# Performance work log

Measured on AMD Instinct MI355X. Metric: run time of the kernel, lower is better.

Reference implementation:

```python
import jax, jax.numpy as jnp
import numpy as np

B, DM, DC, H = 16384, 1024, 8, 256  # batch, MRI feat dim, clinical feat dim, hidden_dim


def setup_inputs() -> dict:
    key = jax.random.key(0)
    ks = jax.random.split(key, 16)
    f = lambda k, s: jax.random.normal(k, s, dtype=jnp.float32)
    return {
        # encoder outputs (4 MRI modalities @1024-d, clinical @8-d)
        'feat_t1': f(ks[0], (B, DM)), 'feat_t1c': f(ks[1], (B, DM)),
        'feat_t2': f(ks[2], (B, DM)), 'feat_flair': f(ks[3], (B, DM)),
        'feat_cl': f(ks[4], (B, DC)),
        # per-modality projection Linears (MRI ones stacked: same math as 4 separate Linears)
        'Wp_mri': f(ks[5], (4, H, DM)) * 0.02, 'bp_mri': jnp.zeros((4, H), jnp.float32),
        'Wp_cl': f(ks[6], (H, DC)) * 0.02, 'bp_cl': jnp.zeros((H,), jnp.float32),
        # attention MLP: Linear(256,64) -> Tanh -> Linear(64,1)
        'Wa1': f(ks[7], (64, H)) * 0.02, 'ba1': jnp.zeros((64,), jnp.float32),
        'Wa2': f(ks[8], (1, 64)) * 0.02, 'ba2': jnp.zeros((1,), jnp.float32),
        # classifier: 256->128 LN ReLU -> 128->64 LN ReLU -> 64->1 (num_class-1)
        'Wc1': f(ks[9], (128, H)) * 0.02, 'bc1': jnp.zeros((128,), jnp.float32),
        'g1': jnp.ones((128,), jnp.float32), 'be1': jnp.zeros((128,), jnp.float32),
        'Wc2': f(ks[10], (64, 128)) * 0.02, 'bc2': jnp.zeros((64,), jnp.float32),
        'g2': jnp.ones((64,), jnp.float32), 'be2': jnp.zeros((64,), jnp.float32),
        'Wc3': f(ks[11], (1, 64)) * 0.02, 'bc3': jnp.zeros((1,), jnp.float32),
    }


def _ln(x, g, b, eps=1e-5):
    m = jnp.mean(x, axis=-1, keepdims=True)
    v = jnp.var(x, axis=-1, keepdims=True)
    return (x - m) * jax.lax.rsqrt(v + eps) * g + b


def reference(feat_t1, feat_t1c, feat_t2, feat_flair, feat_cl,
              Wp_mri, bp_mri, Wp_cl, bp_cl,
              Wa1, ba1, Wa2, ba2,
              Wc1, bc1, g1, be1, Wc2, bc2, g2, be2, Wc3, bc3):
    mri = jnp.stack([feat_t1, feat_t1c, feat_t2, feat_flair], axis=1)  # [B,4,DM]
    pm = jnp.einsum('bmd,mhd->bmh', mri, Wp_mri) + bp_mri              # [B,4,H] per-modality Linear
    pc = feat_cl @ Wp_cl.T + bp_cl                                     # [B,H]
    proj = jnp.concatenate([pm, pc[:, None, :]], axis=1)               # [B,5,H] == torch.stack(proj_feats, dim=1)
    scores = jnp.tanh(proj @ Wa1.T + ba1) @ Wa2.T + ba2                # [B,5,1]
    attn_weights = jax.nn.softmax(scores, axis=1)                      # softmax over modalities
    fused = jnp.sum(attn_weights * proj, axis=1)                       # [B,H]
    h = jax.nn.relu(_ln(fused @ Wc1.T + bc1, g1, be1))                 # dropout is identity in eval
    h = jax.nn.relu(_ln(h @ Wc2.T + bc2, g2, be2))
    out = h @ Wc3.T + bc3                                              # [B,1]
    return out, attn_weights
```

## Files before the change

### kernel.cpp

```cpp
#include <hip/hip_runtime.h>
#include <math.h>

typedef unsigned short u16;
typedef unsigned int   u32;
typedef __bf16 bf16x8 __attribute__((ext_vector_type(8)));
typedef float  f32x4  __attribute__((ext_vector_type(4)));
typedef u16    u16x8  __attribute__((ext_vector_type(8)));
typedef u16    u16x4  __attribute__((ext_vector_type(4)));

#define B_TOT 16384
#define DM_   1024
#define H_    256

#define WS_SCORES 41943040
#define WS_WP     42270720
#define WS_WA1    44367872
#define WS_WC1    44400640
#define WS_WC2    44466176

__device__ __forceinline__ u16 f2bf(float f){
  __bf16 h = (__bf16)f;
  return __builtin_bit_cast(u16, h);
}
__device__ __forceinline__ float bf2f(u16 h){
  return __builtin_bit_cast(float, ((u32)h) << 16);
}
__device__ __forceinline__ u16x4 cvt4(f32x4 a){
  u16x4 h;
  #pragma unroll
  for (int j = 0; j < 4; j++) h[j] = f2bf(a[j]);
  return h;
}
__device__ __forceinline__ f32x4 mfma16(bf16x8 a, bf16x8 b, f32x4 c){
  return __builtin_amdgcn_mfma_f32_16x16x32_bf16(a, b, c, 0, 0, 0);
}
__device__ __forceinline__ void glds16(const void* g, void* l){
  __builtin_amdgcn_global_load_lds(
      (const __attribute__((address_space(1))) void*)g,
      (__attribute__((address_space(3))) void*)l, 16, 0, 0);
}

__global__ void k0_convert(const float* __restrict__ s0, u16* __restrict__ d0, int n0,
                           const float* __restrict__ s1, u16* __restrict__ d1, int n1,
                           const float* __restrict__ s2, u16* __restrict__ d2, int n2,
                           const float* __restrict__ s3, u16* __restrict__ d3, int n3)
{
  int total4 = (n0 + n1 + n2 + n3) >> 2;
  for (int i = blockIdx.x * blockDim.x + threadIdx.x; i < total4; i += gridDim.x * blockDim.x){
    int e = i << 2;
    const float* s; u16* d; int off;
    if (e < n0)            { s = s0; d = d0; off = e; }
    else if (e < n0+n1)    { s = s1; d = d1; off = e - n0; }
    else if (e < n0+n1+n2) { s = s2; d = d2; off = e - n0 - n1; }
    else                   { s = s3; d = d3; off = e - n0 - n1 - n2; }
    f32x4 f = *(const f32x4*)(s + off);
    *(u16x4*)(d + off) = cvt4(f);
  }
}

__global__ __launch_bounds__(256) void k1b_clin(
    const float* __restrict__ fcl, const float* __restrict__ Wpcl, const float* __restrict__ bpcl,
    const u16* __restrict__ Wa1bf, const float* __restrict__ ba1,
    const float* __restrict__ Wa2, const float* __restrict__ ba2,
    u16* __restrict__ proj, float* __restrict__ scores)
{
  __shared__ u16 pcs[4][16*264];
  const int tid = threadIdx.x, lane = tid & 63, wv = tid >> 6;
  const int l15 = lane & 15, l4 = lane >> 4;
  const int rbase = blockIdx.x * 64 + wv * 16;

  f32x4 wA[4], wB[4];
  f32x4 bp = *(const f32x4*)(bpcl + lane * 4);
  #pragma unroll
  for (int c = 0; c < 4; c++){
    wA[c] = *(const f32x4*)(Wpcl + (lane*4 + c) * 8);
    wB[c] = *(const f32x4*)(Wpcl + (lane*4 + c) * 8 + 4);
  }
  #pragma unroll 4
  for (int r = 0; r < 16; r++){
    int row = rbase + r;
    f32x4 fA = *(const f32x4*)(fcl + (size_t)row * 8);
    f32x4 fB = *(const f32x4*)(fcl + (size_t)row * 8 + 4);
    u16x4 h;
    #pragma unroll
    for (int c = 0; c < 4; c++){
      float v = bp[c] + fA[0]*wA[c][0] + fA[1]*wA[c][1] + fA[2]*wA[c][2] + fA[3]*wA[c][3]
                      + fB[0]*wB[c][0] + fB[1]*wB[c][1] + fB[2]*wB[c][2] + fB[3]*wB[c][3];
      h[c] = f2bf(v);
    }
    *(u16x4*)(proj + (size_t)row * 1280 + 1024 + lane * 4) = h;
    *(u16x4*)(&pcs[wv][r * 264 + lane * 4]) = h;
  }
  f32x4 at[4];
  #pragma unroll
  for (int nf = 0; nf < 4; nf++) at[nf] = f32x4{0.f,0.f,0.f,0.f};
  #pragma unroll
  for (int kk = 0; kk < 8; kk++){
    bf16x8 a = *(const bf16x8*)((const char*)&pcs[wv][0] + l15*528 + kk*64 + l4*16);
    #pragma unroll
    for (int nf = 0; nf < 4; nf++){
      bf16x8 b = *(const bf16x8*)((const char*)Wa1bf + (nf*16 + l15)*512 + kk*64 + l4*16);
      at[nf] = mfma16(a, b, at[nf]);
    }
  }
  float po[4] = {0.f,0.f,0.f,0.f};
  #pragma unroll
  for (int nf = 0; nf < 4; nf++){
    int col = nf*16 + l15;
    float bb = ba1[col], w2 = Wa2[col];
    #pragma unroll
    for (int rg = 0; rg < 4; rg++) po[rg] += tanhf(at[nf][rg] + bb) * w2;
  }
  #pragma unroll
  for (int rg = 0; rg < 4; rg++){
    #pragma unroll
    for (int d = 1; d < 16; d <<= 1) po[rg] += __shfl_xor(po[rg], d);
  }
  if (l15 == 0){
    float b2 = ba2[0];
    #pragma unroll
    for (int rg = 0; rg < 4; rg++)
      scores[(size_t)(rbase + l4*4 + rg) * 5 + 4] = po[rg] + b2;
  }
}

__global__ __launch_bounds__(512, 4) void k1_proj(
    const float* __restrict__ ft1, const float* __restrict__ ft1c,
    const float* __restrict__ ft2, const float* __restrict__ ftfl,
    const u16* __restrict__ Wpbf, const float* __restrict__ bpm,
    const u16* __restrict__ Wa1bf, const float* __restrict__ ba1,
    const float* __restrict__ Wa2, const float* __restrict__ ba2,
    u16* __restrict__ proj, float* __restrict__ scores)
{
  extern __shared__ char lds[];
  const int bid = blockIdx.x;
  const int mm = (bid & 7) >> 1;
  const int bx = ((bid >> 3) << 1) | (bid & 1);
  const int b0 = bx * 64;
  const int tid = threadIdx.x;
  const int lane = tid & 63;
  const int wv = tid >> 6;
  const int wm = wv >> 2, wn = wv & 3;
  const int l15 = lane & 15, l4 = lane >> 4;

  const float* Am = (mm == 0) ? ft1 : ((mm == 1) ? ft1c : ((mm == 2) ? ft2 : ftfl));
  const char*  Wm = (const char*)(Wpbf + (size_t)mm * (H_ * DM_));
  const char*  Ab8 = (const char*)Am;

  const int a_r = tid >> 3, a_c = tid & 7;
  const size_t a_src0 = (size_t)(b0 + a_r) * 4096 + (size_t)((a_c*16) ^ ((a_r & 7) << 4));
  const int a_dstw = (tid >> 6) * 1024;
  size_t w_src0[2];
  #pragma unroll
  for (int i = 0; i < 2; i++){
    int q = i*512 + tid; int pr = q >> 3, c = q & 7;
    int zp = (c*16) ^ ((pr & 7) << 4);
    int col = 2*pr + (zp >> 6);
    w_src0[i] = (size_t)col * 2048 + (size_t)(zp & 63);
  }

  f32x4 acc[2][4];
  #pragma unroll
  for (int i = 0; i < 2; i++)
    #pragma unroll
    for (int j = 0; j < 4; j++) acc[i][j] = f32x4{0.f,0.f,0.f,0.f};

  int a_off[2], a_off2[2], w_off[4];
  #pragma unroll
  for (int mf = 0; mf < 2; mf++){
    int r = wm*32 + mf*16 + l15;
    a_off[mf]  = r*128 + ((l4*32) ^ ((r & 7) << 4));
    a_off2[mf] = r*128 + (((l4*32) + 16) ^ ((r & 7) << 4));
  }
  #pragma unroll
  for (int nf = 0; nf < 4; nf++){
    int col = wn*64 + nf*16 + l15;
    int p = col >> 1, qq = col & 1;
    w_off[nf] = p*128 + (((qq*64) + l4*16) ^ ((p & 7) << 4));
  }

  auto stage = [&](int t){
    int bc = t % 3;
    glds16(Ab8 + a_src0 + (size_t)t * 128, lds + bc*8192 + a_dstw);
    #pragma unroll
    for (int i = 0; i < 2; i++)
      glds16(Wm + w_src0[i] + (size_t)t * 64, lds + 24576 + bc*16384 + i*8192 + a_dstw);
  };
  auto compute = [&](int t){
    int bc = t % 3;
    const char* Abuf = lds + bc*8192;
    const char* Wbuf = lds + 24576 + bc*16384;
    bf16x8 af[2];
    #pragma unroll
    for (int mf = 0; mf < 2; mf++){
      f32x4 a0 = *(const f32x4*)(Abuf + a_off[mf]);
      f32x4 a1 = *(const f32x4*)(Abuf + a_off2[mf]);
      bf16x8 h;
      #pragma unroll
      for (int j = 0; j < 4; j++){ h[j] = (__bf16)a0[j]; h[4+j] = (__bf16)a1[j]; }
      af[mf] = h;
    }
    bf16x8 wfr[4];
    #pragma unroll
    for (int nf = 0; nf < 4; nf++) wfr[nf] = *(const bf16x8*)(Wbuf + w_off[nf]);
    __builtin_amdgcn_s_setprio(1);
    #pragma unroll
    for (int nf = 0; nf < 4; nf++){
      #pragma unroll
      for (int mf = 0; mf < 2; mf++)
        acc[mf][nf] = mfma16(af[mf], wfr[nf], acc[mf][nf]);
    }
    __builtin_amdgcn_s_setprio(0);
  };

  stage(0);
  stage(1);

  for (int kt = 0; kt < 31; ++kt){
    asm volatile("s_waitcnt vmcnt(3)" ::: "memory");
    __builtin_amdgcn_s_barrier();
    __builtin_amdgcn_sched_barrier(0);
    if (kt + 2 < 32) stage(kt + 2);
    compute(kt);
  }
  asm volatile("s_waitcnt vmcnt(0)" ::: "memory");
  __builtin_amdgcn_s_barrier();
  __builtin_amdgcn_sched_barrier(0);
  compute(31);

  __syncthreads();

  {
    float bias[4];
    #pragma unroll
    for (int nf = 0; nf < 4; nf++) bias[nf] = bpm[mm*256 + wn*64 + nf*16 + l15];
    #pragma unroll
    for (int mf = 0; mf < 2; mf++){
      #pragma unroll
      for (int nf = 0; nf < 4; nf++){
        int cc = wn*64 + nf*16 + l15;
        #pragma unroll
        for (int rg = 0; rg < 4; rg++){
          int r = wm*32 + mf*16 + l4*4 + rg;
          *(u16*)(lds + r*512 + ((cc*2) ^ ((r & 7) << 4))) = f2bf(acc[mf][nf][rg] + bias[nf]);
        }
      }
    }
  }
  __syncthreads();

  #pragma unroll
  for (int i = 0; i < 4; i++){
    int q = i*512 + tid;
    int r = q >> 5, c = q & 31;
    u16x8 v = *(const u16x8*)(lds + r*512 + ((c*16) ^ ((r & 7) << 4)));
    *(u16x8*)((char*)proj + (size_t)(b0 + r) * 2560 + mm*512 + c*16) = v;
  }
  if (wv < 4){
    f32x4 a2[4];
    #pragma unroll
    for (int nf = 0; nf < 4; nf++) a2[nf] = f32x4{0.f,0.f,0.f,0.f};
    #pragma unroll
    for (int kk = 0; kk < 8; kk++){
      int kb = kk*64 + l4*16;
      int r = wv*16 + l15;
      bf16x8 afr = *(const bf16x8*)(lds + r*512 + (kb ^ ((r & 7) << 4)));
      #pragma unroll
      for (int nf = 0; nf < 4; nf++){
        int n = nf*16 + l15;
        bf16x8 bfr = *(const bf16x8*)((const char*)Wa1bf + n*512 + kb);
        a2[nf] = mfma16(afr, bfr, a2[nf]);
      }
    }
    float p0 = 0.f, p1 = 0.f, p2 = 0.f, p3 = 0.f;
    #pragma unroll
    for (int nf = 0; nf < 4; nf++){
      int n = nf*16 + l15;
      float w2 = Wa2[n], bn = ba1[n];
      p0 += tanhf(a2[nf][0] + bn) * w2;
      p1 += tanhf(a2[nf][1] + bn) * w2;
      p2 += tanhf(a2[nf][2] + bn) * w2;
      p3 += tanhf(a2[nf][3] + bn) * w2;
    }
    #pragma unroll
    for (int d = 1; d < 16; d <<= 1){
      p0 += __shfl_xor(p0, d); p1 += __shfl_xor(p1, d);
      p2 += __shfl_xor(p2, d); p3 += __shfl_xor(p3, d);
    }
    if (l15 == 0){
      float bav = ba2[0];
      int rb = wv*16 + l4*4;
      scores[(size_t)(b0 + rb + 0)*5 + mm] = p0 + bav;
      scores[(size_t)(b0 + rb + 1)*5 + mm] = p1 + bav;
      scores[(size_t)(b0 + rb + 2)*5 + mm] = p2 + bav;
      scores[(size_t)(b0 + rb + 3)*5 + mm] = p3 + bav;
    }
  }
}

__global__ __launch_bounds__(256) void k2_cls(
    const u16* __restrict__ proj, const float* __restrict__ scores,
    const u16* __restrict__ Wc1bf, const u16* __restrict__ Wc2bf,
    const float* __restrict__ bc1, const float* __restrict__ g1, const float* __restrict__ be1,
    const float* __restrict__ bc2, const float* __restrict__ g2, const float* __restrict__ be2,
    const float* __restrict__ Wc3, const float* __restrict__ bc3,
    float* __restrict__ outp)
{
  __shared__ u16 h1s[4][16*136];
  const int tid = threadIdx.x, lane = tid & 63, wv = tid >> 6;
  const int l15 = lane & 15, l4 = lane >> 4;
  const int b0 = blockIdx.x * 64;
  const int rowA = b0 + wv*16 + l15;

  const float* sc = scores + (size_t)rowA * 5;
  float s0 = sc[0], s1 = sc[1], s2 = sc[2], s3 = sc[3], s4 = sc[4];
  float mx = fmaxf(fmaxf(fmaxf(s0, s1), fmaxf(s2, s3)), s4);
  float e0 = expf(s0-mx), e1 = expf(s1-mx), e2 = expf(s2-mx), e3 = expf(s3-mx), e4 = expf(s4-mx);
  float inv = 1.0f / (e0 + e1 + e2 + e3 + e4);
  float w0 = e0*inv, w1 = e1*inv, w2 = e2*inv, w3 = e3*inv, w4 = e4*inv;
  if (l4 == 0){
    float* ap = outp + B_TOT + (size_t)rowA * 5;
    ap[0] = w0; ap[1] = w1; ap[2] = w2; ap[3] = w3; ap[4] = w4;
  }

  bf16x8 af[8];
  const u16* pr = proj + (size_t)rowA * 1280 + l4*8;
  #pragma unroll
  for (int kk = 0; kk < 8; kk++){
    u16x8 p0v = *(const u16x8*)(pr + kk*32);
    u16x8 p1v = *(const u16x8*)(pr + 256  + kk*32);
    u16x8 p2v = *(const u16x8*)(pr + 512  + kk*32);
    u16x8 p3v = *(const u16x8*)(pr + 768  + kk*32);
    u16x8 p4v = *(const u16x8*)(pr + 1024 + kk*32);
    bf16x8 a;
    #pragma unroll
    for (int j = 0; j < 8; j++)
      a[j] = (__bf16)(w0*bf2f(p0v[j]) + w1*bf2f(p1v[j]) + w2*bf2f(p2v[j])
                    + w3*bf2f(p3v[j]) + w4*bf2f(p4v[j]));
    af[kk] = a;
  }

  f32x4 acc1[8];
  #pragma unroll
  for (int of = 0; of < 8; of++) acc1[of] = f32x4{0.f,0.f,0.f,0.f};
  #pragma unroll
  for (int kk = 0; kk < 8; kk++){
    #pragma unroll
    for (int of = 0; of < 8; of++){
      bf16x8 b = *(const bf16x8*)((const char*)Wc1bf + (of*16 + l15)*512 + kk*64 + l4*16);
      acc1[of] = mfma16(af[kk], b, acc1[of]);
    }
  }
  float sum1[4] = {0.f,0.f,0.f,0.f};
  #pragma unroll
  for (int of = 0; of < 8; of++){
    float bb = bc1[of*16 + l15];
    #pragma unroll
    for (int rg = 0; rg < 4; rg++){ acc1[of][rg] += bb; sum1[rg] += acc1[of][rg]; }
  }
  #pragma unroll
  for (int rg = 0; rg < 4; rg++){
    #pragma unroll
    for (int d = 1; d < 16; d <<= 1) sum1[rg] += __shfl_xor(sum1[rg], d);
  }
  float vs1[4] = {0.f,0.f,0.f,0.f};
  float mean1[4];
  #pragma unroll
  for (int rg = 0; rg < 4; rg++) mean1[rg] = sum1[rg] * 0.0078125f;
  #pragma unroll
  for (int of = 0; of < 8; of++)
    #pragma unroll
    for (int rg = 0; rg < 4; rg++){ float dd = acc1[of][rg] - mean1[rg]; vs1[rg] += dd*dd; }
  #pragma unroll
  for (int rg = 0; rg < 4; rg++){
    #pragma unroll
    for (int d = 1; d < 16; d <<= 1) vs1[rg] += __shfl_xor(vs1[rg], d);
  }
  float is1[4];
  #pragma unroll
  for (int rg = 0; rg < 4; rg++) is1[rg] = rsqrtf(vs1[rg] * 0.0078125f + 1e-5f);
  #pragma unroll
  for (int of = 0; of < 8; of++){
    int col = of*16 + l15;
    float gg = g1[col], bb = be1[col];
    #pragma unroll
    for (int rg = 0; rg < 4; rg++){
      float h = fmaxf((acc1[of][rg] - mean1[rg]) * is1[rg] * gg + bb, 0.f);
      h1s[wv][(l4*4 + rg)*136 + col] = f2bf(h);
    }
  }

  f32x4 acc2[4];
  #pragma unroll
  for (int of = 0; of < 4; of++) acc2[of] = f32x4{0.f,0.f,0.f,0.f};
  #pragma unroll
  for (int kk = 0; kk < 4; kk++){
    bf16x8 a2 = *(const bf16x8*)((const char*)&h1s[wv][0] + l15*272 + kk*64 + l4*16);
    #pragma unroll
    for (int of = 0; of < 4; of++){
      bf16x8 b = *(const bf16x8*)((const char*)Wc2bf + (of*16 + l15)*256 + kk*64 + l4*16);
      acc2[of] = mfma16(a2, b, acc2[of]);
    }
  }
  float sum2[4] = {0.f,0.f,0.f,0.f};
  #pragma unroll
  for (int of = 0; of < 4; of++){
    float bb = bc2[of*16 + l15];
    #pragma unroll
    for (int rg = 0; rg < 4; rg++){ acc2[of][rg] += bb; sum2[rg] += acc2[of][rg]; }
  }
  #pragma unroll
  for (int rg = 0; rg < 4; rg++){
    #pragma unroll
    for (int d = 1; d < 16; d <<= 1) sum2[rg] += __shfl_xor(sum2[rg], d);
  }
  float mean2[4], vs2[4] = {0.f,0.f,0.f,0.f};
  #pragma unroll
  for (int rg = 0; rg < 4; rg++) mean2[rg] = sum2[rg] * 0.015625f;
  #pragma unroll
  for (int of = 0; of < 4; of++)
    #pragma unroll
    for (int rg = 0; rg < 4; rg++){ float dd = acc2[of][rg] - mean2[rg]; vs2[rg] += dd*dd; }
  #pragma unroll
  for (int rg = 0; rg < 4; rg++){
    #pragma unroll
    for (int d = 1; d < 16; d <<= 1) vs2[rg] += __shfl_xor(vs2[rg], d);
  }
  float po[4] = {0.f,0.f,0.f,0.f};
  #pragma unroll
  for (int of = 0; of < 4; of++){
    int col = of*16 + l15;
    float gg = g2[col], bb = be2[col], w3c = Wc3[col];
    #pragma unroll
    for (int rg = 0; rg < 4; rg++){
      float is2 = rsqrtf(vs2[rg] * 0.015625f + 1e-5f);
      float h = fmaxf((acc2[of][rg] - mean2[rg]) * is2 * gg + bb, 0.f);
      po[rg] += h * w3c;
    }
  }
  #pragma unroll
  for (int rg = 0; rg < 4; rg++){
    #pragma unroll
    for (int d = 1; d < 16; d <<= 1) po[rg] += __shfl_xor(po[rg], d);
  }
  if (l15 == 0){
    float b3 = bc3[0];
    #pragma unroll
    for (int rg = 0; rg < 4; rg++)
      outp[b0 + wv*16 + l4*4 + rg] = po[rg] + b3;
  }
}

extern "C" void kernel_launch(void* const* d_in, const int* in_sizes, int n_in,
                              void* d_out, int out_size, void* d_ws, size_t ws_size,
                              hipStream_t stream)
{
  (void)in_sizes; (void)n_in; (void)out_size; (void)ws_size;
  const float* ft1  = (const float*)d_in[0];
  const float* ft1c = (const float*)d_in[1];
  const float* ft2  = (const float*)d_in[2];
  const float* ftfl = (const float*)d_in[3];
  const float* fcl  = (const float*)d_in[4];
  const float* Wpmri= (const float*)d_in[5];
  const float* bpm  = (const float*)d_in[6];
  const float* Wpcl = (const float*)d_in[7];
  const float* bpcl = (const float*)d_in[8];
  const float* Wa1  = (const float*)d_in[9];
  const float* ba1  = (const float*)d_in[10];
  const float* Wa2  = (const float*)d_in[11];
  const float* ba2  = (const float*)d_in[12];
  const float* Wc1  = (const float*)d_in[13];
  const float* bc1  = (const float*)d_in[14];
  const float* g1   = (const float*)d_in[15];
  const float* be1  = (const float*)d_in[16];
  const float* Wc2  = (const float*)d_in[17];
  const float* bc2  = (const float*)d_in[18];
  const float* g2   = (const float*)d_in[19];
  const float* be2  = (const float*)d_in[20];
  const float* Wc3  = (const float*)d_in[21];
  const float* bc3  = (const float*)d_in[22];
  float* outp = (float*)d_out;
  char* ws = (char*)d_ws;

  u16*   proj   = (u16*)(ws);
  float* scores = (float*)(ws + WS_SCORES);
  u16*   Wpbf   = (u16*)(ws + WS_WP);
  u16*   Wa1bf  = (u16*)(ws + WS_WA1);
  u16*   Wc1bf  = (u16*)(ws + WS_WC1);
  u16*   Wc2bf  = (u16*)(ws + WS_WC2);

  (void)hipFuncSetAttribute((const void*)k1_proj, hipFuncAttributeMaxDynamicSharedMemorySize, 73728);

  k0_convert<<<dim3(512), dim3(256), 0, stream>>>(
      Wpmri, Wpbf, 4 * H_ * DM_,
      Wa1,  Wa1bf, 64 * H_,
      Wc1,  Wc1bf, 128 * H_,
      Wc2,  Wc2bf, 64 * 128);

  k1b_clin<<<dim3(256), dim3(256), 0, stream>>>(
      fcl, Wpcl, bpcl, Wa1bf, ba1, Wa2, ba2, proj, scores);

  k1_proj<<<dim3(1024), dim3(512), 73728, stream>>>(
      ft1, ft1c, ft2, ftfl, Wpbf, bpm, Wa1bf, ba1, Wa2, ba2, proj, scores);

  k2_cls<<<dim3(256), dim3(256), 0, stream>>>(
      proj, scores, Wc1bf, Wc2bf, bc1, g1, be1, bc2, g2, be2, Wc3, bc3, outp);
}
```

Before: 141.6 us.

## Restructure projection GEMM to register-prefetch A directly and stage W via LDS

The projection kernel drops the async global-to-LDS copies and its triple buffering. Activations are now loaded straight from global memory into registers two K-chunks ahead. Weights go through registers into a double-buffered, swizzled LDS tile, and the block shrinks from 512 to 256 threads, each warp covering 128 output columns. The aim is to cut LDS traffic for the fp32 activations, which are only used by one warp row, and to raise per-warp MFMA work. The cost is higher register pressure and possibly lower occupancy. The epilogue is adjusted to the new warp layout, and all four waves now run the attention-score MFMA.

```diff
diff --git a/kernel.cpp b/kernel.cpp
--- a/kernel.cpp
+++ b/kernel.cpp
@@ -33,11 +33,6 @@
 }
 __device__ __forceinline__ f32x4 mfma16(bf16x8 a, bf16x8 b, f32x4 c){
   return __builtin_amdgcn_mfma_f32_16x16x32_bf16(a, b, c, 0, 0, 0);
-}
-__device__ __forceinline__ void glds16(const void* g, void* l){
-  __builtin_amdgcn_global_load_lds(
-      (const __attribute__((address_space(1))) void*)g,
-      (__attribute__((address_space(3))) void*)l, 16, 0, 0);
 }
 
 __global__ void k0_convert(const float* __restrict__ s0, u16* __restrict__ d0, int n0,
@@ -124,7 +119,7 @@
   }
 }
 
-__global__ __launch_bounds__(512, 4) void k1_proj(
+__global__ __launch_bounds__(256, 2) void k1_proj(
     const float* __restrict__ ft1, const float* __restrict__ ft1c,
     const float* __restrict__ ft2, const float* __restrict__ ftfl,
     const u16* __restrict__ Wpbf, const float* __restrict__ bpm,
@@ -140,105 +135,101 @@
   const int tid = threadIdx.x;
   const int lane = tid & 63;
   const int wv = tid >> 6;
-  const int wm = wv >> 2, wn = wv & 3;
+  const int wm = wv >> 1, wn = wv & 1;
   const int l15 = lane & 15, l4 = lane >> 4;
+  const int sw = (l15 & 7) << 4;
 
   const float* Am = (mm == 0) ? ft1 : ((mm == 1) ? ft1c : ((mm == 2) ? ft2 : ftfl));
-  const char*  Wm = (const char*)(Wpbf + (size_t)mm * (H_ * DM_));
-  const char*  Ab8 = (const char*)Am;
-
-  const int a_r = tid >> 3, a_c = tid & 7;
-  const size_t a_src0 = (size_t)(b0 + a_r) * 4096 + (size_t)((a_c*16) ^ ((a_r & 7) << 4));
-  const int a_dstw = (tid >> 6) * 1024;
-  size_t w_src0[2];
-  #pragma unroll
-  for (int i = 0; i < 2; i++){
-    int q = i*512 + tid; int pr = q >> 3, c = q & 7;
-    int zp = (c*16) ^ ((pr & 7) << 4);
-    int col = 2*pr + (zp >> 6);
-    w_src0[i] = (size_t)col * 2048 + (size_t)(zp & 63);
-  }
-
-  f32x4 acc[2][4];
+  const u16*   Wm = Wpbf + (size_t)mm * (H_ * DM_);
+
+  const float* pA0 = Am + (size_t)(b0 + wm*32 +  0 + l15) * DM_ + l4*8;
+  const float* pA1 = Am + (size_t)(b0 + wm*32 + 16 + l15) * DM_ + l4*8;
+  const u16* pW = Wm + (size_t)tid * DM_;
+
+  u16x8 rW[8];
+  f32x4 rA[2][8];
+  f32x4 acc[2][8];
   #pragma unroll
   for (int i = 0; i < 2; i++)
     #pragma unroll
-    for (int j = 0; j < 4; j++) acc[i][j] = f32x4{0.f,0.f,0.f,0.f};
-
-  int a_off[2], a_off2[2], w_off[4];
-  #pragma unroll
-  for (int mf = 0; mf < 2; mf++){
-    int r = wm*32 + mf*16 + l15;
-    a_off[mf]  = r*128 + ((l4*32) ^ ((r & 7) << 4));
-    a_off2[mf] = r*128 + (((l4*32) + 16) ^ ((r & 7) << 4));
-  }
-  #pragma unroll
-  for (int nf = 0; nf < 4; nf++){
-    int col = wn*64 + nf*16 + l15;
-    int p = col >> 1, qq = col & 1;
-    w_off[nf] = p*128 + (((qq*64) + l4*16) ^ ((p & 7) << 4));
-  }
-
-  auto stage = [&](int t){
-    int bc = t % 3;
-    glds16(Ab8 + a_src0 + (size_t)t * 128, lds + bc*8192 + a_dstw);
-    #pragma unroll
-    for (int i = 0; i < 2; i++)
-      glds16(Wm + w_src0[i] + (size_t)t * 64, lds + 24576 + bc*16384 + i*8192 + a_dstw);
+    for (int j = 0; j < 8; j++) acc[i][j] = f32x4{0.f,0.f,0.f,0.f};
+
+  auto issueW = [&](int c){
+    #pragma unroll
+    for (int i = 0; i < 8; i++) rW[i] = *(const u16x8*)(pW + c*64 + i*8);
   };
-  auto compute = [&](int t){
-    int bc = t % 3;
-    const char* Abuf = lds + bc*8192;
-    const char* Wbuf = lds + 24576 + bc*16384;
+  auto writeW = [&](int c){
+    char* base = lds + (c & 1) * 32768 + tid * 128;
+    #pragma unroll
+    for (int i = 0; i < 8; i++)
+      *(u16x8*)(base + ((i*16) ^ ((tid & 7) << 4))) = rW[i];
+  };
+  auto issueA = [&](int c, int kk){
+    const int p = c & 1;
+    const float* pa0 = pA0 + c*64 + kk*32;
+    const float* pa1 = pA1 + c*64 + kk*32;
+    rA[p][kk*4 + 0] = *(const f32x4*)(pa0);
+    rA[p][kk*4 + 1] = *(const f32x4*)(pa0 + 4);
+    rA[p][kk*4 + 2] = *(const f32x4*)(pa1);
+    rA[p][kk*4 + 3] = *(const f32x4*)(pa1 + 4);
+  };
+  auto computeKK = [&](int c, int kk, bool reload){
+    const int p = c & 1;
     bf16x8 af[2];
     #pragma unroll
     for (int mf = 0; mf < 2; mf++){
-      f32x4 a0 = *(const f32x4*)(Abuf + a_off[mf]);
-      f32x4 a1 = *(const f32x4*)(Abuf + a_off2[mf]);
+      f32x4 a0 = rA[p][kk*4 + mf*2];
+      f32x4 a1 = rA[p][kk*4 + mf*2 + 1];
       bf16x8 h;
       #pragma unroll
       for (int j = 0; j < 4; j++){ h[j] = (__bf16)a0[j]; h[4+j] = (__bf16)a1[j]; }
       af[mf] = h;
     }
-    bf16x8 wfr[4];
-    #pragma unroll
-    for (int nf = 0; nf < 4; nf++) wfr[nf] = *(const bf16x8*)(Wbuf + w_off[nf]);
-    __builtin_amdgcn_s_setprio(1);
-    #pragma unroll
-    for (int nf = 0; nf < 4; nf++){
+    if (reload) issueA(c + 2, kk);
+    const char* rb = lds + (c & 1) * 32768 + wn * 16384 + l15 * 128;
+    #pragma unroll
+    for (int nf = 0; nf < 8; nf++){
+      bf16x8 wf = *(const bf16x8*)(rb + nf*2048 + ((kk*64 + l4*16) ^ sw));
       #pragma unroll
       for (int mf = 0; mf < 2; mf++)
-        acc[mf][nf] = mfma16(af[mf], wfr[nf], acc[mf][nf]);
-    }
-    __builtin_amdgcn_s_setprio(0);
+        acc[mf][nf] = mfma16(af[mf], wf, acc[mf][nf]);
+    }
   };
 
-  stage(0);
-  stage(1);
-
-  for (int kt = 0; kt < 31; ++kt){
-    asm volatile("s_waitcnt vmcnt(3)" ::: "memory");
+  issueW(0);
+  issueA(0, 0); issueA(0, 1);
+  writeW(0);
+  issueW(1);
+  issueA(1, 0); issueA(1, 1);
+  asm volatile("s_waitcnt lgkmcnt(0)" ::: "memory");
+  __builtin_amdgcn_sched_barrier(0);
+  __builtin_amdgcn_s_barrier();
+  __builtin_amdgcn_sched_barrier(0);
+
+  #pragma unroll
+  for (int c = 0; c < 16; ++c){
+    if (c + 1 < 16) writeW(c + 1);
+    if (c + 2 < 16) issueW(c + 2);
+    const bool reload = (c + 2 < 16);
+    computeKK(c, 0, reload);
+    computeKK(c, 1, reload);
+    asm volatile("s_waitcnt lgkmcnt(0)" ::: "memory");
+    __builtin_amdgcn_sched_barrier(0);
     __builtin_amdgcn_s_barrier();
     __builtin_amdgcn_sched_barrier(0);
-    if (kt + 2 < 32) stage(kt + 2);
-    compute(kt);
-  }
-  asm volatile("s_waitcnt vmcnt(0)" ::: "memory");
-  __builtin_amdgcn_s_barrier();
-  __builtin_amdgcn_sched_barrier(0);
-  compute(31);
+  }
 
   __syncthreads();
 
   {
-    float bias[4];
-    #pragma unroll
-    for (int nf = 0; nf < 4; nf++) bias[nf] = bpm[mm*256 + wn*64 + nf*16 + l15];
+    float bias[8];
+    #pragma unroll
+    for (int nf = 0; nf < 8; nf++) bias[nf] = bpm[mm*256 + wn*128 + nf*16 + l15];
     #pragma unroll
     for (int mf = 0; mf < 2; mf++){
       #pragma unroll
-      for (int nf = 0; nf < 4; nf++){
-        int cc = wn*64 + nf*16 + l15;
+      for (int nf = 0; nf < 8; nf++){
+        int cc = wn*128 + nf*16 + l15;
         #pragma unroll
         for (int rg = 0; rg < 4; rg++){
           int r = wm*32 + mf*16 + l4*4 + rg;
@@ -250,13 +241,13 @@
   __syncthreads();
 
   #pragma unroll
-  for (int i = 0; i < 4; i++){
-    int q = i*512 + tid;
-    int r = q >> 5, c = q & 31;
-    u16x8 v = *(const u16x8*)(lds + r*512 + ((c*16) ^ ((r & 7) << 4)));
-    *(u16x8*)((char*)proj + (size_t)(b0 + r) * 2560 + mm*512 + c*16) = v;
-  }
-  if (wv < 4){
+  for (int i = 0; i < 8; i++){
+    int q = i*256 + tid;
+    int r = q >> 5, cc = q & 31;
+    u16x8 v = *(const u16x8*)(lds + r*512 + ((cc*16) ^ ((r & 7) << 4)));
+    *(u16x8*)((char*)proj + (size_t)(b0 + r) * 2560 + mm*512 + cc*16) = v;
+  }
+  {
     f32x4 a2[4];
     #pragma unroll
     for (int nf = 0; nf < 4; nf++) a2[nf] = f32x4{0.f,0.f,0.f,0.f};
@@ -489,7 +480,7 @@
   u16*   Wc1bf  = (u16*)(ws + WS_WC1);
   u16*   Wc2bf  = (u16*)(ws + WS_WC2);
 
-  (void)hipFuncSetAttribute((const void*)k1_proj, hipFuncAttributeMaxDynamicSharedMemorySize, 73728);
+  (void)hipFuncSetAttribute((const void*)k1_proj, hipFuncAttributeMaxDynamicSharedMemorySize, 65536);
 
   k0_convert<<<dim3(512), dim3(256), 0, stream>>>(
       Wpmri, Wpbf, 4 * H_ * DM_,
@@ -500,7 +491,7 @@
   k1b_clin<<<dim3(256), dim3(256), 0, stream>>>(
       fcl, Wpcl, bpcl, Wa1bf, ba1, Wa2, ba2, proj, scores);
 
-  k1_proj<<<dim3(1024), dim3(512), 73728, stream>>>(
+  k1_proj<<<dim3(1024), dim3(256), 65536, stream>>>(
       ft1, ft1c, ft2, ftfl, Wpbf, bpm, Wa1bf, ba1, Wa2, ba2, proj, scores);
 
   k2_cls<<<dim3(256), dim3(256), 0, stream>>>(
```

Result: slower. 194.5 us (+37.4%).
